# Performance work log

Measured on AMD Instinct MI355X. Metric: run time of the kernel, lower is better.

Reference implementation:

```python
import jax, jax.numpy as jnp
import numpy as np

WS = 10      # window_size
HID = 32     # hidden_dim
B, T = 1024, 4096


def setup_inputs() -> dict:
    key = jax.random.key(0)
    k = jax.random.split(key, 7)
    returns = jax.random.normal(k[0], (B, T), dtype=jnp.float32) * 0.01
    W1 = jax.random.normal(k[1], (WS, HID), dtype=jnp.float32) * (1.0 / np.sqrt(WS))
    b1 = jnp.zeros((HID,), dtype=jnp.float32)
    W2 = jax.random.normal(k[2], (HID, HID), dtype=jnp.float32) * (1.0 / np.sqrt(HID))
    b2 = jnp.zeros((HID,), dtype=jnp.float32)
    W3 = jax.random.normal(k[3], (HID, 1), dtype=jnp.float32) * (1.0 / np.sqrt(HID))
    b3 = jnp.zeros((1,), dtype=jnp.float32)
    return {"returns": returns, "W1": W1, "b1": b1, "W2": W2, "b2": b2, "W3": W3, "b3": b3}


def reference(returns, W1, b1, W2, b2, W3, b3):
    ws = W1.shape[0]
    Bb, Tt = returns.shape
    # Unfold all sliding windows at once: windows[b, i, :] = returns[b, i:i+ws]
    # (window ending just before timestep t = i + ws)
    idx = jnp.arange(Tt - ws)[:, None] + jnp.arange(ws)[None, :]  # [T-ws, ws]
    windows = returns[:, idx]                                     # [B, T-ws, ws]
    h = jax.nn.relu(windows @ W1 + b1)                            # [B, T-ws, HID]
    h = jax.nn.relu(h @ W2 + b2)                                  # [B, T-ws, HID]
    out = 0.5 * jax.nn.sigmoid((h @ W3 + b3).squeeze(-1))         # [B, T-ws]
    # H_local[:, t] = out[:, t-ws] for t >= ws; first ws columns copy column ws
    head = jnp.broadcast_to(out[:, :1], (Bb, ws))                 # [B, ws]
    return jnp.concatenate([head, out], axis=1)                   # [B, T]
```

## Files before the change

kernel.cpp:

```cpp
#include <hip/hip_runtime.h>
#include <math.h>

typedef _Float16 f16x8  __attribute__((ext_vector_type(8)));
typedef float    f32x16 __attribute__((ext_vector_type(16)));
typedef __fp16   h2a    __attribute__((ext_vector_type(2)));
typedef unsigned u32x4  __attribute__((ext_vector_type(4)));

#define WS    10
#define HID   32
#define BDIM  256
#define NWAVE 4
#define GN    32
#define TILE  1024
#define NGRP  (TILE / GN)

__device__ inline unsigned pack2u(float a, float b) {
    h2a t = __builtin_amdgcn_cvt_pkrtz(a, b);
    return __builtin_bit_cast(unsigned, t);
}

__global__ __launch_bounds__(BDIM, 2)
void hurst_mlp_mfma32(const float* __restrict__ returns,
                      const float* __restrict__ W1, const float* __restrict__ b1,
                      const float* __restrict__ W2, const float* __restrict__ b2,
                      const float* __restrict__ W3, const float* __restrict__ b3,
                      float* __restrict__ out, int T)
{
    __shared__ float sret[TILE + WS];
    __shared__ __align__(16) _Float16 Xh[TILE][16];

    const int tid  = threadIdx.x;
    const int wid  = tid >> 6;
    const int lane = tid & 63;
    const int n    = lane & 31;
    const int hi   = lane >> 5;
    const int permidx = (lane ^ 32) << 2;

    f32x16 b1v, b2v, w3v;
    #pragma unroll
    for (int r = 0; r < 16; ++r) {
        const int rw = (r & 3) + 8 * (r >> 2) + 4 * hi;
        b1v[r] = b1[rw];
        b2v[r] = b2[rw];
        w3v[r] = W3[rw];
    }
    const float b3s = b3[0];

    f16x8 a1, a2lo, a2hi;
    #pragma unroll
    for (int jj = 0; jj < 8; ++jj) {
        const int k = 8 * hi + jj;
        a1[jj]   = (k < WS) ? (_Float16)W1[k * HID + n] : (_Float16)0.0f;
        a2lo[jj] = (_Float16)W2[k * HID + n];
        a2hi[jj] = (_Float16)W2[(16 + k) * HID + n];
    }

    const int    b    = blockIdx.y;
    const int    t0   = blockIdx.x * TILE;
    const int    base = (t0 >= WS) ? (t0 - WS) : 0;
    const size_t row  = (size_t)b * (size_t)T;

    for (int i = tid; i < TILE + WS; i += BDIM) {
        int g = base + i;
        sret[i] = (g < T) ? returns[row + g] : 0.0f;
    }
    __syncthreads();

    #pragma unroll
    for (int i = 0; i < TILE / BDIM; ++i) {
        const int m   = tid + i * BDIM;
        const int t   = t0 + m;
        const int off = (t >= WS) ? (t - WS - base) : 0;
        u32x4 lo, hi4;
        lo[0]  = pack2u(sret[off + 0], sret[off + 1]);
        lo[1]  = pack2u(sret[off + 2], sret[off + 3]);
        lo[2]  = pack2u(sret[off + 4], sret[off + 5]);
        lo[3]  = pack2u(sret[off + 6], sret[off + 7]);
        hi4[0] = pack2u(sret[off + 8], sret[off + 9]);
        hi4[1] = 0u; hi4[2] = 0u; hi4[3] = 0u;
        *(u32x4*)&Xh[m][0] = lo;
        *(u32x4*)&Xh[m][8] = hi4;
    }
    __syncthreads();

    for (int g = wid; g < NGRP; g += NWAVE) {
        const int m0 = g * GN;

        const f16x8 xb = *(const f16x8*)&Xh[m0 + n][hi * 8];
        f32x16 d1 = b1v;
        d1 = __builtin_amdgcn_mfma_f32_32x32x16_f16(a1, xb, d1, 0, 0, 0);

        unsigned pk[8];
        #pragma unroll
        for (int i = 0; i < 8; ++i)
            pk[i] = pack2u(fmaxf(d1[2 * i], 0.0f), fmaxf(d1[2 * i + 1], 0.0f));

        const unsigned s0 = hi ? pk[0] : pk[2];
        const unsigned s1 = hi ? pk[1] : pk[3];
        const unsigned s2 = hi ? pk[4] : pk[6];
        const unsigned s3 = hi ? pk[5] : pk[7];
        const unsigned q0 = (unsigned)__builtin_amdgcn_ds_bpermute(permidx, (int)s0);
        const unsigned q1 = (unsigned)__builtin_amdgcn_ds_bpermute(permidx, (int)s1);
        const unsigned q2 = (unsigned)__builtin_amdgcn_ds_bpermute(permidx, (int)s2);
        const unsigned q3 = (unsigned)__builtin_amdgcn_ds_bpermute(permidx, (int)s3);
        u32x4 blo_u, bhi_u;
        blo_u[0] = hi ? q0    : pk[0];
        blo_u[1] = hi ? q1    : pk[1];
        blo_u[2] = hi ? pk[2] : q0;
        blo_u[3] = hi ? pk[3] : q1;
        bhi_u[0] = hi ? q2    : pk[4];
        bhi_u[1] = hi ? q3    : pk[5];
        bhi_u[2] = hi ? pk[6] : q2;
        bhi_u[3] = hi ? pk[7] : q3;
        const f16x8 blo = __builtin_bit_cast(f16x8, blo_u);
        const f16x8 bhi = __builtin_bit_cast(f16x8, bhi_u);

        f32x16 d2 = b2v;
        d2 = __builtin_amdgcn_mfma_f32_32x32x16_f16(a2lo, blo, d2, 0, 0, 0);
        d2 = __builtin_amdgcn_mfma_f32_32x32x16_f16(a2hi, bhi, d2, 0, 0, 0);

        float acc = 0.0f;
        #pragma unroll
        for (int r = 0; r < 16; ++r)
            acc = fmaf(fmaxf(d2[r], 0.0f), w3v[r], acc);
        const int pai = __builtin_amdgcn_ds_bpermute(permidx, __builtin_bit_cast(int, acc));
        acc += __builtin_bit_cast(float, pai);

        const float v = acc + b3s;
        const float o = 0.5f * __builtin_amdgcn_rcpf(1.0f + __expf(-v));
        if (hi == 0)
            out[row + (size_t)(t0 + m0 + n)] = o;
    }
}

extern "C" void kernel_launch(void* const* d_in, const int* in_sizes, int n_in,
                              void* d_out, int out_size, void* d_ws, size_t ws_size,
                              hipStream_t stream) {
    const float* returns = (const float*)d_in[0];
    const float* W1      = (const float*)d_in[1];
    const float* b1      = (const float*)d_in[2];
    const float* W2      = (const float*)d_in[3];
    const float* b2      = (const float*)d_in[4];
    const float* W3      = (const float*)d_in[5];
    const float* b3      = (const float*)d_in[6];
    float* out = (float*)d_out;

    const int T = 4096;
    const int B = out_size / T;

    dim3 grid(T / TILE, B, 1);
    dim3 block(BDIM, 1, 1);
    hurst_mlp_mfma32<<<grid, block, 0, stream>>>(returns, W1, b1, W2, b2, W3, b3, out, T);
}
```

Baseline: 116.1 us.

## Permute W2 rows so layer-1 MFMA output feeds layer-2 directly without bpermute

Reorders the K dimension of the W2 A-operand so that each lane's layer-1 accumulator registers, once packed to fp16, already form the B operand for the layer-2 MFMAs. This removes four ds_bpermute cross-lane exchanges and the select logic per 32-row group. It also loads bias and W3 vectors with 128-bit loads and software-prefetches the next group's LDS input before the current group's MFMAs. Correctness depends on the permuted K mapping matching the MFMA output register layout exactly.

```diff
diff --git a/kernel.cpp b/kernel.cpp
--- a/kernel.cpp
+++ b/kernel.cpp
@@ -3,6 +3,7 @@
 
 typedef _Float16 f16x8  __attribute__((ext_vector_type(8)));
 typedef float    f32x16 __attribute__((ext_vector_type(16)));
+typedef float    f32x4  __attribute__((ext_vector_type(4)));
 typedef __fp16   h2a    __attribute__((ext_vector_type(2)));
 typedef unsigned u32x4  __attribute__((ext_vector_type(4)));
 
@@ -20,11 +21,11 @@
 }
 
 __global__ __launch_bounds__(BDIM, 2)
-void hurst_mlp_mfma32(const float* __restrict__ returns,
-                      const float* __restrict__ W1, const float* __restrict__ b1,
-                      const float* __restrict__ W2, const float* __restrict__ b2,
-                      const float* __restrict__ W3, const float* __restrict__ b3,
-                      float* __restrict__ out, int T)
+void hurst_mlp_mfma32v2(const float* __restrict__ returns,
+                        const float* __restrict__ W1, const float* __restrict__ b1,
+                        const float* __restrict__ W2, const float* __restrict__ b2,
+                        const float* __restrict__ W3, const float* __restrict__ b3,
+                        float* __restrict__ out, int T)
 {
     __shared__ float sret[TILE + WS];
     __shared__ __align__(16) _Float16 Xh[TILE][16];
@@ -38,21 +39,27 @@
 
     f32x16 b1v, b2v, w3v;
     #pragma unroll
-    for (int r = 0; r < 16; ++r) {
-        const int rw = (r & 3) + 8 * (r >> 2) + 4 * hi;
-        b1v[r] = b1[rw];
-        b2v[r] = b2[rw];
-        w3v[r] = W3[rw];
+    for (int i = 0; i < 4; ++i) {
+        const f32x4 v1 = ((const f32x4*)b1)[2 * i + hi];
+        const f32x4 v2 = ((const f32x4*)b2)[2 * i + hi];
+        const f32x4 v3 = ((const f32x4*)W3)[2 * i + hi];
+        #pragma unroll
+        for (int o = 0; o < 4; ++o) {
+            b1v[4 * i + o] = v1[o];
+            b2v[4 * i + o] = v2[o];
+            w3v[4 * i + o] = v3[o];
+        }
     }
     const float b3s = b3[0];
 
     f16x8 a1, a2lo, a2hi;
     #pragma unroll
     for (int jj = 0; jj < 8; ++jj) {
-        const int k = 8 * hi + jj;
-        a1[jj]   = (k < WS) ? (_Float16)W1[k * HID + n] : (_Float16)0.0f;
-        a2lo[jj] = (_Float16)W2[k * HID + n];
-        a2hi[jj] = (_Float16)W2[(16 + k) * HID + n];
+        const int k  = 8 * hi + jj;
+        a1[jj] = (k < WS) ? (_Float16)W1[k * HID + n] : (_Float16)0.0f;
+        const int kf = (k & 3) | ((k & 4) << 1) | ((k & 8) >> 1);
+        a2lo[jj] = (_Float16)W2[kf * HID + n];
+        a2hi[jj] = (_Float16)W2[(16 + kf) * HID + n];
     }
 
     const int    b    = blockIdx.y;
@@ -83,53 +90,37 @@
     }
     __syncthreads();
 
+    f16x8 xb = *(const f16x8*)&Xh[wid * GN + n][hi * 8];
     for (int g = wid; g < NGRP; g += NWAVE) {
-        const int m0 = g * GN;
+        const int gn = (g + NWAVE < NGRP) ? (g + NWAVE) : g;
+        const f16x8 xb_next = *(const f16x8*)&Xh[gn * GN + n][hi * 8];
 
-        const f16x8 xb = *(const f16x8*)&Xh[m0 + n][hi * 8];
         f32x16 d1 = b1v;
         d1 = __builtin_amdgcn_mfma_f32_32x32x16_f16(a1, xb, d1, 0, 0, 0);
 
-        unsigned pk[8];
+        u32x4 blo_u, bhi_u;
         #pragma unroll
-        for (int i = 0; i < 8; ++i)
-            pk[i] = pack2u(fmaxf(d1[2 * i], 0.0f), fmaxf(d1[2 * i + 1], 0.0f));
-
-        const unsigned s0 = hi ? pk[0] : pk[2];
-        const unsigned s1 = hi ? pk[1] : pk[3];
-        const unsigned s2 = hi ? pk[4] : pk[6];
-        const unsigned s3 = hi ? pk[5] : pk[7];
-        const unsigned q0 = (unsigned)__builtin_amdgcn_ds_bpermute(permidx, (int)s0);
-        const unsigned q1 = (unsigned)__builtin_amdgcn_ds_bpermute(permidx, (int)s1);
-        const unsigned q2 = (unsigned)__builtin_amdgcn_ds_bpermute(permidx, (int)s2);
-        const unsigned q3 = (unsigned)__builtin_amdgcn_ds_bpermute(permidx, (int)s3);
-        u32x4 blo_u, bhi_u;
-        blo_u[0] = hi ? q0    : pk[0];
-        blo_u[1] = hi ? q1    : pk[1];
-        blo_u[2] = hi ? pk[2] : q0;
-        blo_u[3] = hi ? pk[3] : q1;
-        bhi_u[0] = hi ? q2    : pk[4];
-        bhi_u[1] = hi ? q3    : pk[5];
-        bhi_u[2] = hi ? pk[6] : q2;
-        bhi_u[3] = hi ? pk[7] : q3;
-        const f16x8 blo = __builtin_bit_cast(f16x8, blo_u);
-        const f16x8 bhi = __builtin_bit_cast(f16x8, bhi_u);
+        for (int i = 0; i < 4; ++i) {
+            blo_u[i] = pack2u(fmaxf(d1[2 * i],     0.0f), fmaxf(d1[2 * i + 1], 0.0f));
+            bhi_u[i] = pack2u(fmaxf(d1[8 + 2 * i], 0.0f), fmaxf(d1[9 + 2 * i], 0.0f));
+        }
 
         f32x16 d2 = b2v;
-        d2 = __builtin_amdgcn_mfma_f32_32x32x16_f16(a2lo, blo, d2, 0, 0, 0);
-        d2 = __builtin_amdgcn_mfma_f32_32x32x16_f16(a2hi, bhi, d2, 0, 0, 0);
+        d2 = __builtin_amdgcn_mfma_f32_32x32x16_f16(a2lo, __builtin_bit_cast(f16x8, blo_u), d2, 0, 0, 0);
+        d2 = __builtin_amdgcn_mfma_f32_32x32x16_f16(a2hi, __builtin_bit_cast(f16x8, bhi_u), d2, 0, 0, 0);
 
         float acc = 0.0f;
         #pragma unroll
         for (int r = 0; r < 16; ++r)
             acc = fmaf(fmaxf(d2[r], 0.0f), w3v[r], acc);
-        const int pai = __builtin_amdgcn_ds_bpermute(permidx, __builtin_bit_cast(int, acc));
-        acc += __builtin_bit_cast(float, pai);
+        acc += __builtin_bit_cast(float,
+                 __builtin_amdgcn_ds_bpermute(permidx, __builtin_bit_cast(int, acc)));
 
-        const float v = acc + b3s;
-        const float o = 0.5f * __builtin_amdgcn_rcpf(1.0f + __expf(-v));
+        const float o = 0.5f * __builtin_amdgcn_rcpf(1.0f + __expf(-(acc + b3s)));
         if (hi == 0)
-            out[row + (size_t)(t0 + m0 + n)] = o;
+            out[row + (size_t)(t0 + g * GN + n)] = o;
+
+        xb = xb_next;
     }
 }
 
@@ -150,5 +141,5 @@
 
     dim3 grid(T / TILE, B, 1);
     dim3 block(BDIM, 1, 1);
-    hurst_mlp_mfma32<<<grid, block, 0, stream>>>(returns, W1, b1, W2, b2, W3, b3, out, T);
+    hurst_mlp_mfma32v2<<<grid, block, 0, stream>>>(returns, W1, b1, W2, b2, W3, b3, out, T);
 }
```

Result: faster. 113.0 us (-2.7%).
